# Kernel tuning notes

Hardware: AMD Instinct MI355X
Metric: run time of the kernel (lower is better)

The kernel has to match this reference:

```python
import jax, jax.numpy as jnp
import numpy as np

N_NODES = 100000
N_EDGES = 1600000
IN_DIM = 64
HIDDEN = 64
N_CLASSES = 249


def sage_conv(x, edge_index, W_l, b_l, W_r):
    # PyG SAGEConv with aggr='add': out = lin_l(sum_{j->i} x_j) + lin_r(x_i)
    src, dst = edge_index[0], edge_index[1]
    msgs = x[src]                                   # [E, d] gather
    agg = jax.ops.segment_sum(msgs, dst, num_segments=x.shape[0])  # [N, d]
    return agg @ W_l.T + b_l + x @ W_r.T


def setup_inputs() -> dict:
    key = jax.random.key(0)
    ks = jax.random.split(key, 8)
    x = jax.random.normal(ks[0], (N_NODES, IN_DIM), dtype=jnp.float32)
    edge_index = jax.random.randint(ks[1], (2, N_EDGES), 0, N_NODES, dtype=jnp.int64 if jax.config.jax_enable_x64 else jnp.int32)
    s1 = 1.0 / np.sqrt(IN_DIM)
    s2 = 1.0 / np.sqrt(HIDDEN)
    W1_l = jax.random.uniform(ks[2], (HIDDEN, IN_DIM), jnp.float32, -s1, s1)
    b1_l = jax.random.uniform(ks[3], (HIDDEN,), jnp.float32, -s1, s1)
    W1_r = jax.random.uniform(ks[4], (HIDDEN, IN_DIM), jnp.float32, -s1, s1)
    W2_l = jax.random.uniform(ks[5], (N_CLASSES, HIDDEN), jnp.float32, -s2, s2)
    b2_l = jax.random.uniform(ks[6], (N_CLASSES,), jnp.float32, -s2, s2)
    W2_r = jax.random.uniform(ks[7], (N_CLASSES, HIDDEN), jnp.float32, -s2, s2)
    return {"x": x, "edge_index": edge_index, "W1_l": W1_l, "b1_l": b1_l,
            "W1_r": W1_r, "W2_l": W2_l, "b2_l": b2_l, "W2_r": W2_r}


def reference(x, edge_index, W1_l, b1_l, W1_r, W2_l, b2_l, W2_r):
    h = sage_conv(x, edge_index, W1_l, b1_l, W1_r)
    h = jax.nn.relu(h)
    # dropout p=0.5 is identity at inference (training=False)
    out = sage_conv(h, edge_index, W2_l, b2_l, W2_r)
    return out
```

## Files before the change

### kernel.cpp

```cpp
#include <hip/hip_runtime.h>

#define DIM 64
#define NCLS 249
#define SCAN_CHUNK 1024
#define NCHUNK 192
#define PSHIFT 7
#define PSIZE 128
#define SBITS 17
#define SMASK ((1u << SBITS) - 1)
#define MAXP 1024

typedef unsigned int u32;
typedef unsigned short u16;
using bf16x8 = __attribute__((ext_vector_type(8))) short;
using f32x4  = __attribute__((ext_vector_type(4))) float;

__device__ __forceinline__ u16 f2bf(float f) {
    u32 u = __builtin_bit_cast(u32, f);
    u += 0x7FFFu + ((u >> 16) & 1u);
    return (u16)(u >> 16);
}
__device__ __forceinline__ float bf_lo(u32 u) { return __builtin_bit_cast(float, u << 16); }
__device__ __forceinline__ float bf_hi(u32 u) { return __builtin_bit_cast(float, u & 0xFFFF0000u); }

__global__ __launch_bounds__(256) void build_kernel(
    const int* __restrict__ dst, int E, int chunk_size, int nxp,
    int* __restrict__ bcnt,
    const float* __restrict__ x, u16* __restrict__ A1, int nx8,
    const float* __restrict__ W1l, const float* __restrict__ W1r, u16* __restrict__ B1,
    const float* __restrict__ W2l, const float* __restrict__ W2r, u16* __restrict__ B2)
{
    __shared__ int c[MAXP];
    int t = threadIdx.x;
    if (blockIdx.x < NCHUNK) {
        for (int i = t; i < nxp; i += 256) c[i] = 0;
        __syncthreads();
        int base = blockIdx.x * chunk_size;
        int end = min(base + chunk_size, E);
        for (int e = base + t; e < end; e += 256) {
            int d = __builtin_nontemporal_load(&dst[e]);
            atomicAdd(&c[d >> PSHIFT], 1);
        }
        __syncthreads();
        for (int i = t; i < nxp; i += 256) bcnt[i * NCHUNK + blockIdx.x] = c[i];
        return;
    }
    int i = (blockIdx.x - NCHUNK) * 256 + t;
    if (i < nx8) {
        int node = i >> 3, seg = i & 7;
        const float4 v0 = *(const float4*)(x + (size_t)i * 8);
        const float4 v1 = *(const float4*)(x + (size_t)i * 8 + 4);
        uint4 o;
        o.x = (u32)f2bf(v0.x) | ((u32)f2bf(v0.y) << 16);
        o.y = (u32)f2bf(v0.z) | ((u32)f2bf(v0.w) << 16);
        o.z = (u32)f2bf(v1.x) | ((u32)f2bf(v1.y) << 16);
        o.w = (u32)f2bf(v1.z) | ((u32)f2bf(v1.w) << 16);
        *(uint4*)(A1 + (size_t)node * 128 + 64 + seg * 8) = o;
        return;
    }
    int j = i - nx8;
    if (j < 64 * 128) {
        int r = j >> 7, k = j & 127;
        B1[j] = f2bf(k < 64 ? W1l[r * 64 + k] : W1r[r * 64 + k - 64]);
        return;
    }
    j -= 64 * 128;
    if (j < 256 * 128) {
        int r = j >> 7, k = j & 127;
        float v = 0.f;
        if (r < NCLS) v = (k < 64) ? W2l[r * 64 + k] : W2r[r * 64 + k - 64];
        B2[j] = f2bf(v);
    }
}

__global__ __launch_bounds__(256) void scan_block_sums(const int* __restrict__ cnt, int n,
                                                       int* __restrict__ bsum) {
    __shared__ int sdata[256];
    int b = blockIdx.x, t = threadIdx.x;
    int base = b * SCAN_CHUNK;
    int s = 0;
    for (int i = t; i < SCAN_CHUNK; i += 256) {
        int idx = base + i;
        s += (idx < n) ? cnt[idx] : 0;
    }
    sdata[t] = s;
    __syncthreads();
    for (int off = 128; off > 0; off >>= 1) {
        if (t < off) sdata[t] += sdata[t + off];
        __syncthreads();
    }
    if (t == 0) bsum[b] = sdata[0];
}

__global__ __launch_bounds__(256) void scan_final_boff(const int* __restrict__ cnt, int n,
                                                       const int* __restrict__ bsum_raw, int nb,
                                                       int* __restrict__ boff, int total) {
    __shared__ int bpre[256];
    __shared__ int tsum[256];
    int b = blockIdx.x, t = threadIdx.x;
    int bv = (t < nb) ? bsum_raw[t] : 0;
    bpre[t] = bv;
    __syncthreads();
    for (int off = 1; off < 256; off <<= 1) {
        int u = (t >= off) ? bpre[t - off] : 0;
        __syncthreads();
        bpre[t] += u;
        __syncthreads();
    }
    int block_base = (b == 0) ? 0 : bpre[b - 1];
    int base = b * SCAN_CHUNK + t * 4;
    int v[4];
    int s = 0;
#pragma unroll
    for (int i = 0; i < 4; ++i) {
        int id = base + i;
        v[i] = (id < n) ? cnt[id] : 0;
        s += v[i];
    }
    tsum[t] = s;
    __syncthreads();
    for (int off = 1; off < 256; off <<= 1) {
        int u = (t >= off) ? tsum[t - off] : 0;
        __syncthreads();
        tsum[t] += u;
        __syncthreads();
    }
    int run = tsum[t] - s + block_base;
#pragma unroll
    for (int i = 0; i < 4; ++i) {
        int id = base + i;
        if (id < n) boff[id] = run;
        run += v[i];
    }
    if (b == 0 && t == 0) boff[n] = total;
}

__global__ __launch_bounds__(256) void bucket_scatter(const int* __restrict__ ei, int E,
                                                      int chunk_size, int nxp,
                                                      const int* __restrict__ boff,
                                                      u32* __restrict__ bucket) {
    __shared__ int cur[MAXP];
    int t = threadIdx.x;
    for (int i = t; i < nxp; i += 256) cur[i] = boff[i * NCHUNK + blockIdx.x];
    __syncthreads();
    int base = blockIdx.x * chunk_size;
    int end = min(base + chunk_size, E);
    for (int e = base + t; e < end; e += 256) {
        int s = __builtin_nontemporal_load(&ei[e]);
        int d = __builtin_nontemporal_load(&ei[E + e]);
        int pos = atomicAdd(&cur[d >> PSHIFT], 1);
        bucket[pos] = ((u32)(d & (PSIZE - 1)) << SBITS) | (u32)s;
    }
}

__global__ __launch_bounds__(256) void sort_bucket(const u32* __restrict__ bucket,
                                                   const int* __restrict__ boff,
                                                   int* __restrict__ nbr,
                                                   int* __restrict__ row_ptr,
                                                   int n, int E) {
    __shared__ int cnt[PSIZE];
    __shared__ int sc[PSIZE];
    __shared__ int cur[PSIZE];
    int t = threadIdx.x;
    int p = blockIdx.x;
    if (t < PSIZE) cnt[t] = 0;
    __syncthreads();
    int beg = boff[p * NCHUNK];
    int end = boff[(p + 1) * NCHUNK];
    for (int i = beg + t; i < end; i += 256)
        atomicAdd(&cnt[bucket[i] >> SBITS], 1);
    __syncthreads();
    if (t < PSIZE) sc[t] = cnt[t];
    __syncthreads();
    for (int off = 1; off < PSIZE; off <<= 1) {
        int v = 0;
        if (t < PSIZE && t >= off) v = sc[t - off];
        __syncthreads();
        if (t < PSIZE) sc[t] += v;
        __syncthreads();
    }
    if (t < PSIZE) {
        int excl = beg + sc[t] - cnt[t];
        cur[t] = excl;
        int node = p * PSIZE + t;
        if (node < n) row_ptr[node] = excl;
    }
    if (p == 0 && t == 0) row_ptr[n] = E;
    __syncthreads();
    for (int i = beg + t; i < end; i += 256) {
        u32 pk = bucket[i];
        int pos = atomicAdd(&cur[pk >> SBITS], 1);
        nbr[pos] = (int)(pk & SMASK);
    }
}

__global__ __launch_bounds__(256) void pull_bf16(const u16* __restrict__ Asrc,
                                                 const int* __restrict__ row_ptr,
                                                 const int* __restrict__ nbr,
                                                 u16* __restrict__ Adst, int n) {
    int tid = blockIdx.x * 256 + threadIdx.x;
    int node = tid >> 3;
    int q = tid & 7;
    if (node >= n) return;
    int beg = row_ptr[node], end = row_ptr[node + 1];
    float a0 = 0.f, a1 = 0.f, a2 = 0.f, a3 = 0.f, a4 = 0.f, a5 = 0.f, a6 = 0.f, a7 = 0.f;
    int myj = beg + q;
    int snext = (myj < end) ? nbr[myj] : 0;
    for (int j0 = beg; j0 < end; j0 += 8) {
        int smine = snext;
        myj = j0 + 8 + q;
        snext = (myj < end) ? nbr[myj] : 0;
        int cnt = min(8, end - j0);
#pragma unroll 4
        for (int k = 0; k < cnt; ++k) {
            int s = __shfl(smine, k, 8);
            uint4 v = *(const uint4*)(Asrc + (size_t)s * 128 + 64 + q * 8);
            a0 += bf_lo(v.x); a1 += bf_hi(v.x);
            a2 += bf_lo(v.y); a3 += bf_hi(v.y);
            a4 += bf_lo(v.z); a5 += bf_hi(v.z);
            a6 += bf_lo(v.w); a7 += bf_hi(v.w);
        }
    }
    uint4 o;
    o.x = (u32)f2bf(a0) | ((u32)f2bf(a1) << 16);
    o.y = (u32)f2bf(a2) | ((u32)f2bf(a3) << 16);
    o.z = (u32)f2bf(a4) | ((u32)f2bf(a5) << 16);
    o.w = (u32)f2bf(a6) | ((u32)f2bf(a7) << 16);
    *(uint4*)(Adst + (size_t)node * 128 + q * 8) = o;
}

template<int NT, bool RELU, bool OUT_BF16>
__global__ __launch_bounds__(256) void gemm_kernel(
    const u16* __restrict__ A, const u16* __restrict__ B,
    const float* __restrict__ bias,
    float* __restrict__ outf, u16* __restrict__ outb,
    int n_nodes, int n_cols)
{
    constexpr int KC = (NT == 16) ? 2 : 1;
    constexpr int KW = 128 / KC;
    constexpr int RG = KW / 8;
    constexpr int NR = NT * 16;
    __shared__ uint4 smem[3072];
    uint4* A_lds = smem;
    uint4* B_lds = smem + 1024;

    const int t = threadIdx.x;
    const int node0 = blockIdx.x * 64;

#pragma unroll
    for (int i = 0; i < 4; ++i) {
        int gl = t + 256 * i;
        int r = gl >> 4, g = gl & 15;
        uint4 v = make_uint4(0u, 0u, 0u, 0u);
        int node = node0 + r;
        if (node < n_nodes) v = *(const uint4*)(A + (size_t)node * 128 + g * 8);
        A_lds[r * 16 + (g ^ (r & 7))] = v;
    }

    const int w  = t >> 6;
    const int l  = t & 63;
    const int lm = l & 15;
    const int lg = l >> 4;
    const int arow = w * 16 + lm;
    const int asw  = arow & 7;

    f32x4 acc[NT];
#pragma unroll
    for (int n = 0; n < NT; ++n) acc[n] = f32x4{0.f, 0.f, 0.f, 0.f};

#pragma unroll
    for (int kc = 0; kc < KC; ++kc) {
        __syncthreads();
#pragma unroll
        for (int i = 0; i < (NR * RG) / 256; ++i) {
            int gl = t + 256 * i;
            int r = gl / RG, g = gl % RG;
            uint4 v = *(const uint4*)(B + (size_t)r * 128 + kc * KW + g * 8);
            B_lds[r * RG + (g ^ (r & 7))] = v;
        }
        __syncthreads();
#pragma unroll
        for (int ks = 0; ks < KW / 32; ++ks) {
            int ag = lg + (kc * (KW / 32) + ks) * 4;
            bf16x8 af = __builtin_bit_cast(bf16x8, A_lds[arow * 16 + (ag ^ asw)]);
#pragma unroll
            for (int n = 0; n < NT; ++n) {
                int brow = n * 16 + lm;
                int bg = lg + ks * 4;
                bf16x8 bf = __builtin_bit_cast(bf16x8, B_lds[brow * RG + (bg ^ (brow & 7))]);
                acc[n] = __builtin_amdgcn_mfma_f32_16x16x32_bf16(af, bf, acc[n], 0, 0, 0);
            }
        }
    }

    if (OUT_BF16) {
        const int rbase = w * 16 + lg * 4;
#pragma unroll
        for (int n = 0; n < NT; ++n) {
            int c = n * 16 + lm;
            float bv = (c < n_cols) ? bias[c] : 0.f;
#pragma unroll
            for (int r = 0; r < 4; ++r) {
                int node = node0 + rbase + r;
                if (node < n_nodes && c < n_cols) {
                    float v = acc[n][r] + bv;
                    if (RELU) v = fmaxf(v, 0.f);
                    outb[(size_t)node * 128 + 64 + c] = f2bf(v);
                }
            }
        }
    } else {
        float bc[NT];
#pragma unroll
        for (int n = 0; n < NT; ++n) {
            int c = n * 16 + lm;
            bc[n] = (c < n_cols) ? bias[c] : 0.f;
        }
        float* S = reinterpret_cast<float*>(smem);
        __syncthreads();
#pragma unroll
        for (int rc = 0; rc < 2; ++rc) {
            if (rc) __syncthreads();
            if ((lg >> 1) == rc) {
                int lrow = (lg & 1) * 4;
                float* Sw = S + ((size_t)w * 8 + lrow) * 264;
#pragma unroll
                for (int n = 0; n < NT; ++n) {
#pragma unroll
                    for (int r = 0; r < 4; ++r) {
                        float v = acc[n][r] + bc[n];
                        if (RELU) v = fmaxf(v, 0.f);
                        Sw[r * 264 + n * 16 + lm] = v;
                    }
                }
            }
            __syncthreads();
            const float* Sw = S + (size_t)w * 8 * 264;
#pragma unroll
            for (int row8 = 0; row8 < 8; ++row8) {
                int node = node0 + w * 16 + rc * 8 + row8;
                if (node >= n_nodes) continue;
                float* orow = outf + (size_t)node * (size_t)n_cols;
#pragma unroll
                for (int k = 0; k < 4; ++k) {
                    int c = k * 64 + l;
                    if (c < n_cols) orow[c] = Sw[row8 * 264 + c];
                }
            }
        }
    }
}

extern "C" void kernel_launch(void* const* d_in, const int* in_sizes, int n_in,
                              void* d_out, int out_size, void* d_ws, size_t ws_size,
                              hipStream_t stream) {
    const float* x   = (const float*)d_in[0];
    const int*   ei  = (const int*)d_in[1];
    const float* W1l = (const float*)d_in[2];
    const float* b1  = (const float*)d_in[3];
    const float* W1r = (const float*)d_in[4];
    const float* W2l = (const float*)d_in[5];
    const float* b2  = (const float*)d_in[6];
    const float* W2r = (const float*)d_in[7];
    float* out = (float*)d_out;

    const int N = in_sizes[0] / DIM;
    const int E = in_sizes[1] / 2;
    const int NPAD = ((N + 63) / 64) * 64;
    const int NXP = (N + PSIZE - 1) / PSIZE;
    const int NSC = NXP * NCHUNK;
    const int NB2 = (NSC + SCAN_CHUNK - 1) / SCAN_CHUNK;

    char* wp = (char*)d_ws;
    u16* A1 = (u16*)wp;                 wp += (size_t)NPAD * 128 * 2;
    u16* A2 = (u16*)wp;                 wp += (size_t)NPAD * 128 * 2;
    u16* B1 = (u16*)wp;                 wp += 64 * 128 * 2;
    u16* B2 = (u16*)wp;                 wp += 256 * 128 * 2;
    int* bcnt = (int*)wp;               wp += (size_t)NSC * 4;
    int* boff = (int*)wp;               wp += (size_t)(NSC + 1) * 4;
    int* bsum = (int*)wp;               wp += 1024 * 4;
    int* row_ptr = (int*)wp;            wp += (size_t)(N + 1) * 4;
    u32* bucket = (u32*)wp;             wp += (size_t)E * 4;
    int* nbr = (int*)wp;                wp += (size_t)E * 4;

    const int chunk_size = (E + NCHUNK - 1) / NCHUNK;
    const int nx8 = N * 8;
    const int prep_items = nx8 + 64 * 128 + 256 * 128;
    const int prep_blocks = (prep_items + 255) / 256;

    build_kernel<<<NCHUNK + prep_blocks, 256, 0, stream>>>(
        ei + E, E, chunk_size, NXP, bcnt, x, A1, nx8, W1l, W1r, B1, W2l, W2r, B2);

    scan_block_sums<<<NB2, 256, 0, stream>>>(bcnt, NSC, bsum);
    scan_final_boff<<<NB2, 256, 0, stream>>>(bcnt, NSC, bsum, NB2, boff, E);

    bucket_scatter<<<NCHUNK, 256, 0, stream>>>(ei, E, chunk_size, NXP, boff, bucket);
    sort_bucket<<<NXP, 256, 0, stream>>>(bucket, boff, nbr, row_ptr, N, E);

    const int gemm_blocks = NPAD / 64;

    pull_bf16<<<(nx8 + 255) / 256, 256, 0, stream>>>(A1, row_ptr, nbr, A1, N);
    gemm_kernel<4, true, true><<<gemm_blocks, 256, 0, stream>>>(A1, B1, b1, nullptr, A2, N, 64);

    pull_bf16<<<(nx8 + 255) / 256, 256, 0, stream>>>(A2, row_ptr, nbr, A2, N);
    gemm_kernel<16, false, false><<<gemm_blocks, 256, 0, stream>>>(A2, B2, b2, out, nullptr, N, NCLS);
}
```

Before: 197.4 us.

## Split layer-2 GEMM across column halves and fully unroll full pull chunks

```diff
diff --git a/kernel.cpp b/kernel.cpp
--- a/kernel.cpp
+++ b/kernel.cpp
@@ -210,15 +210,26 @@
         int smine = snext;
         myj = j0 + 8 + q;
         snext = (myj < end) ? nbr[myj] : 0;
-        int cnt = min(8, end - j0);
-#pragma unroll 4
-        for (int k = 0; k < cnt; ++k) {
-            int s = __shfl(smine, k, 8);
-            uint4 v = *(const uint4*)(Asrc + (size_t)s * 128 + 64 + q * 8);
-            a0 += bf_lo(v.x); a1 += bf_hi(v.x);
-            a2 += bf_lo(v.y); a3 += bf_hi(v.y);
-            a4 += bf_lo(v.z); a5 += bf_hi(v.z);
-            a6 += bf_lo(v.w); a7 += bf_hi(v.w);
+        if (j0 + 8 <= end) {
+#pragma unroll
+            for (int k = 0; k < 8; ++k) {
+                int s = __shfl(smine, k, 8);
+                uint4 v = *(const uint4*)(Asrc + (size_t)s * 128 + 64 + q * 8);
+                a0 += bf_lo(v.x); a1 += bf_hi(v.x);
+                a2 += bf_lo(v.y); a3 += bf_hi(v.y);
+                a4 += bf_lo(v.z); a5 += bf_hi(v.z);
+                a6 += bf_lo(v.w); a7 += bf_hi(v.w);
+            }
+        } else {
+            int cnt = end - j0;
+            for (int k = 0; k < cnt; ++k) {
+                int s = __shfl(smine, k, 8);
+                uint4 v = *(const uint4*)(Asrc + (size_t)s * 128 + 64 + q * 8);
+                a0 += bf_lo(v.x); a1 += bf_hi(v.x);
+                a2 += bf_lo(v.y); a3 += bf_hi(v.y);
+                a4 += bf_lo(v.z); a5 += bf_hi(v.z);
+                a6 += bf_lo(v.w); a7 += bf_hi(v.w);
+            }
         }
     }
     uint4 o;
@@ -229,20 +240,13 @@
     *(uint4*)(Adst + (size_t)node * 128 + q * 8) = o;
 }
 
-template<int NT, bool RELU, bool OUT_BF16>
-__global__ __launch_bounds__(256) void gemm_kernel(
+__global__ __launch_bounds__(256) void gemm1_kernel(
     const u16* __restrict__ A, const u16* __restrict__ B,
-    const float* __restrict__ bias,
-    float* __restrict__ outf, u16* __restrict__ outb,
-    int n_nodes, int n_cols)
+    const float* __restrict__ bias, u16* __restrict__ outb, int n_nodes)
 {
-    constexpr int KC = (NT == 16) ? 2 : 1;
-    constexpr int KW = 128 / KC;
-    constexpr int RG = KW / 8;
-    constexpr int NR = NT * 16;
-    __shared__ uint4 smem[3072];
-    uint4* A_lds = smem;
-    uint4* B_lds = smem + 1024;
+    constexpr int NT = 4;
+    __shared__ uint4 A_lds[1024];
+    __shared__ uint4 B_lds[1024];
 
     const int t = threadIdx.x;
     const int node0 = blockIdx.x * 64;
@@ -256,6 +260,12 @@
         if (node < n_nodes) v = *(const uint4*)(A + (size_t)node * 128 + g * 8);
         A_lds[r * 16 + (g ^ (r & 7))] = v;
     }
+#pragma unroll
+    for (int i = 0; i < 4; ++i) {
+        int gl = t + 256 * i;
+        int r = gl >> 4, g = gl & 15;
+        B_lds[r * 16 + (g ^ (r & 7))] = *(const uint4*)(B + (size_t)r * 128 + g * 8);
+    }
 
     const int w  = t >> 6;
     const int l  = t & 63;
@@ -268,84 +278,121 @@
 #pragma unroll
     for (int n = 0; n < NT; ++n) acc[n] = f32x4{0.f, 0.f, 0.f, 0.f};
 
-#pragma unroll
-    for (int kc = 0; kc < KC; ++kc) {
-        __syncthreads();
-#pragma unroll
-        for (int i = 0; i < (NR * RG) / 256; ++i) {
-            int gl = t + 256 * i;
-            int r = gl / RG, g = gl % RG;
-            uint4 v = *(const uint4*)(B + (size_t)r * 128 + kc * KW + g * 8);
-            B_lds[r * RG + (g ^ (r & 7))] = v;
-        }
-        __syncthreads();
-#pragma unroll
-        for (int ks = 0; ks < KW / 32; ++ks) {
-            int ag = lg + (kc * (KW / 32) + ks) * 4;
-            bf16x8 af = __builtin_bit_cast(bf16x8, A_lds[arow * 16 + (ag ^ asw)]);
+    __syncthreads();
+#pragma unroll
+    for (int ks = 0; ks < 4; ++ks) {
+        int ag = lg + ks * 4;
+        bf16x8 af = __builtin_bit_cast(bf16x8, A_lds[arow * 16 + (ag ^ asw)]);
+#pragma unroll
+        for (int n = 0; n < NT; ++n) {
+            int brow = n * 16 + lm;
+            bf16x8 bf = __builtin_bit_cast(bf16x8, B_lds[brow * 16 + (ag ^ (brow & 7))]);
+            acc[n] = __builtin_amdgcn_mfma_f32_16x16x32_bf16(af, bf, acc[n], 0, 0, 0);
+        }
+    }
+
+    const int rbase = w * 16 + lg * 4;
+#pragma unroll
+    for (int n = 0; n < NT; ++n) {
+        int c = n * 16 + lm;
+        float bv = bias[c];
+#pragma unroll
+        for (int r = 0; r < 4; ++r) {
+            int node = node0 + rbase + r;
+            if (node < n_nodes) {
+                float v = fmaxf(acc[n][r] + bv, 0.f);
+                outb[(size_t)node * 128 + 64 + c] = f2bf(v);
+            }
+        }
+    }
+}
+
+__global__ __launch_bounds__(256) void gemm2_kernel(
+    const u16* __restrict__ A, const u16* __restrict__ B,
+    const float* __restrict__ bias, float* __restrict__ outf, int n_nodes)
+{
+    constexpr int NT = 8;
+    __shared__ uint4 smem[3072];
+    uint4* A_lds = smem;
+    uint4* B_lds = smem + 1024;
+
+    const int t = threadIdx.x;
+    const int node0 = blockIdx.x * 64;
+    const int cbase = blockIdx.y * 128;
+
+#pragma unroll
+    for (int i = 0; i < 4; ++i) {
+        int gl = t + 256 * i;
+        int r = gl >> 4, g = gl & 15;
+        uint4 v = make_uint4(0u, 0u, 0u, 0u);
+        int node = node0 + r;
+        if (node < n_nodes) v = *(const uint4*)(A + (size_t)node * 128 + g * 8);
+        A_lds[r * 16 + (g ^ (r & 7))] = v;
+    }
+#pragma unroll
+    for (int i = 0; i < 8; ++i) {
+        int gl = t + 256 * i;
+        int r = gl >> 4, g = gl & 15;
+        B_lds[r * 16 + (g ^ (r & 7))] = *(const uint4*)(B + (size_t)(cbase + r) * 128 + g * 8);
+    }
+
+    const int w  = t >> 6;
+    const int l  = t & 63;
+    const int lm = l & 15;
+    const int lg = l >> 4;
+    const int arow = w * 16 + lm;
+    const int asw  = arow & 7;
+
+    f32x4 acc[NT];
+#pragma unroll
+    for (int n = 0; n < NT; ++n) acc[n] = f32x4{0.f, 0.f, 0.f, 0.f};
+
+    __syncthreads();
+#pragma unroll
+    for (int ks = 0; ks < 4; ++ks) {
+        int ag = lg + ks * 4;
+        bf16x8 af = __builtin_bit_cast(bf16x8, A_lds[arow * 16 + (ag ^ asw)]);
+#pragma unroll
+        for (int n = 0; n < NT; ++n) {
+            int brow = n * 16 + lm;
+            bf16x8 bf = __builtin_bit_cast(bf16x8, B_lds[brow * 16 + (ag ^ (brow & 7))]);
+            acc[n] = __builtin_amdgcn_mfma_f32_16x16x32_bf16(af, bf, acc[n], 0, 0, 0);
+        }
+    }
+
+    float bc[NT];
+#pragma unroll
+    for (int n = 0; n < NT; ++n) {
+        int c = cbase + n * 16 + lm;
+        bc[n] = (c < NCLS) ? bias[c] : 0.f;
+    }
+    float* S = reinterpret_cast<float*>(smem);
+    __syncthreads();
+#pragma unroll
+    for (int rc = 0; rc < 2; ++rc) {
+        if (rc) __syncthreads();
+        if ((lg >> 1) == rc) {
+            int lrow = (lg & 1) * 4;
+            float* Sw = S + ((size_t)w * 8 + lrow) * 132;
 #pragma unroll
             for (int n = 0; n < NT; ++n) {
-                int brow = n * 16 + lm;
-                int bg = lg + ks * 4;
-                bf16x8 bf = __builtin_bit_cast(bf16x8, B_lds[brow * RG + (bg ^ (brow & 7))]);
-                acc[n] = __builtin_amdgcn_mfma_f32_16x16x32_bf16(af, bf, acc[n], 0, 0, 0);
-            }
-        }
-    }
-
-    if (OUT_BF16) {
-        const int rbase = w * 16 + lg * 4;
-#pragma unroll
-        for (int n = 0; n < NT; ++n) {
-            int c = n * 16 + lm;
-            float bv = (c < n_cols) ? bias[c] : 0.f;
-#pragma unroll
-            for (int r = 0; r < 4; ++r) {
-                int node = node0 + rbase + r;
-                if (node < n_nodes && c < n_cols) {
-                    float v = acc[n][r] + bv;
-                    if (RELU) v = fmaxf(v, 0.f);
-                    outb[(size_t)node * 128 + 64 + c] = f2bf(v);
+#pragma unroll
+                for (int r = 0; r < 4; ++r) {
+                    Sw[r * 132 + n * 16 + lm] = acc[n][r] + bc[n];
                 }
             }
         }
-    } else {
-        float bc[NT];
-#pragma unroll
-        for (int n = 0; n < NT; ++n) {
-            int c = n * 16 + lm;
-            bc[n] = (c < n_cols) ? bias[c] : 0.f;
-        }
-        float* S = reinterpret_cast<float*>(smem);
-        __syncthreads();
-#pragma unroll
-        for (int rc = 0; rc < 2; ++rc) {
-            if (rc) __syncthreads();
-            if ((lg >> 1) == rc) {
-                int lrow = (lg & 1) * 4;
-                float* Sw = S + ((size_t)w * 8 + lrow) * 264;
-#pragma unroll
-                for (int n = 0; n < NT; ++n) {
-#pragma unroll
-                    for (int r = 0; r < 4; ++r) {
-                        float v = acc[n][r] + bc[n];
-                        if (RELU) v = fmaxf(v, 0.f);
-                        Sw[r * 264 + n * 16 + lm] = v;
-                    }
-                }
-            }
-            __syncthreads();
-            const float* Sw = S + (size_t)w * 8 * 264;
-#pragma unroll
-            for (int row8 = 0; row8 < 8; ++row8) {
-                int node = node0 + w * 16 + rc * 8 + row8;
-                if (node >= n_nodes) continue;
-                float* orow = outf + (size_t)node * (size_t)n_cols;
-#pragma unroll
-                for (int k = 0; k < 4; ++k) {
-                    int c = k * 64 + l;
-                    if (c < n_cols) orow[c] = Sw[row8 * 264 + c];
-                }
+        __syncthreads();
+        const float* Sw = S + (size_t)w * 8 * 132;
+#pragma unroll
+        for (int row8 = 0; row8 < 8; ++row8) {
+            int node = node0 + w * 16 + rc * 8 + row8;
+            if (node >= n_nodes) continue;
+            float* orow = outf + (size_t)node * NCLS + cbase;
+#pragma unroll
+            for (int k = 0; k < 2; ++k) {
+                int c = k * 64 + l;
+                if (cbase + c < NCLS) orow[c] = Sw[row8 * 132 + c];
             }
         }
     }
@@ -400,8 +447,8 @@
     const int gemm_blocks = NPAD / 64;
 
     pull_bf16<<<(nx8 + 255) / 256, 256, 0, stream>>>(A1, row_ptr, nbr, A1, N);
-    gemm_kernel<4, true, true><<<gemm_blocks, 256, 0, stream>>>(A1, B1, b1, nullptr, A2, N, 64);
+    gemm1_kernel<<<gemm_blocks, 256, 0, stream>>>(A1, B1, b1, A2, N);
 
     pull_bf16<<<(nx8 + 255) / 256, 256, 0, stream>>>(A2, row_ptr, nbr, A2, N);
-    gemm_kernel<16, false, false><<<gemm_blocks, 256, 0, stream>>>(A2, B2, b2, out, nullptr, N, NCLS);
-}
+    gemm2_kernel<<<dim3(gemm_blocks, 2), 256, 0, stream>>>(A2, B2, b2, out, N);
+}
```

New measurement: 192.0 us. 2.7% less time.
